# Kernel tuning notes

Measured on AMD Instinct MI355X. Metric: run time of the kernel, lower is better.

Reference implementation:

```python
import jax, jax.numpy as jnp
import numpy as np

N = 20000      # num_nodes
E = 320000     # num_edges (avg degree 16)
HID = 256      # hid_dim
H = 4          # attention heads
D = HID // H   # per-head dim (concat heads -> HID)
L = 2          # nGAT_layer
OUT = 12       # out_dim / pred_len (decoder steps)
NEG_SLOPE = 0.2


def setup_inputs() -> dict:
    key = jax.random.key(0)
    ks = jax.random.split(key, 16)
    s = 0.05
    nrm = lambda k, shape: jax.random.normal(k, shape, jnp.float32) * s
    return dict(
        x=nrm(ks[0], (N, HID)),
        edge_index=jax.random.randint(ks[1], (2, E), 0, N, dtype=jnp.int32),
        # GATv2Conv params per layer (stacked over L layers)
        gat_w_src=nrm(ks[2], (L, HID, H * D)),
        gat_w_dst=nrm(ks[3], (L, HID, H * D)),
        gat_att=nrm(ks[4], (L, H, D)),
        gat_bias=nrm(ks[5], (L, H * D)),
        # decoder_mlp: Linear(1 + HID -> HID)
        mlp_w=nrm(ks[6], (HID, 1 + HID)),
        mlp_b=nrm(ks[7], (HID,)),
        # nn.LSTM (1 layer, input HID, hidden HID), torch gate order i,f,g,o
        lstm_w_ih=nrm(ks[8], (4 * HID, HID)),
        lstm_w_hh=nrm(ks[9], (4 * HID, HID)),
        lstm_b_ih=nrm(ks[10], (4 * HID,)),
        lstm_b_hh=nrm(ks[11], (4 * HID,)),
        # decoder_init_proj: Linear(HID -> 1); decoder_output_proj: Linear(HID -> 1)
        init_w=nrm(ks[12], (1, HID)),
        init_b=nrm(ks[13], (1,)),
        out_w=nrm(ks[14], (1, HID)),
        out_b=nrm(ks[15], (1,)),
    )


def _gatv2_layer(x, src, dst, w_src, w_dst, att, bias):
    n = x.shape[0]
    xl = (x @ w_src).reshape(n, H, D)   # source-side projection
    xr = (x @ w_dst).reshape(n, H, D)   # destination-side projection
    # GATv2: e_ij = a^T LeakyReLU(Wl x_j + Wr x_i)
    e = jax.nn.leaky_relu(xl[src] + xr[dst], NEG_SLOPE)        # [E,H,D]
    logits = jnp.einsum('ehd,hd->eh', e, att)                   # [E,H]
    # edge softmax over incoming edges of each destination node
    m = jax.ops.segment_max(logits, dst, num_segments=n)        # [N,H]
    ex = jnp.exp(logits - m[dst])
    denom = jax.ops.segment_sum(ex, dst, num_segments=n)
    alpha = ex / denom[dst]                                     # [E,H]
    out = jax.ops.segment_sum(xl[src] * alpha[:, :, None], dst, num_segments=n)
    return out.reshape(n, H * D) + bias


def reference(x, edge_index, gat_w_src, gat_w_dst, gat_att, gat_bias,
              mlp_w, mlp_b, lstm_w_ih, lstm_w_hh, lstm_b_ih, lstm_b_hh,
              init_w, init_b, out_w, out_b):
    src, dst = edge_index[0], edge_index[1]
    # stacked GAT blocks: GATv2Conv + ELU (element == 2)
    for l in range(L):
        x = _gatv2_layer(x, src, dst, gat_w_src[l], gat_w_dst[l], gat_att[l], gat_bias[l])
        x = jax.nn.elu(x)
    # recurrent LSTM decoder, batch = nodes, seq step by step
    ctx = x                      # encoder_context
    h = x                        # h_0 = x (num_layers = 1)
    c = jnp.zeros_like(x)        # c_0 = 0
    prev = x @ init_w.T + init_b  # [N,1]
    outs = []
    for _ in range(OUT):
        dec_in = jnp.concatenate([prev, ctx], axis=1) @ mlp_w.T + mlp_b  # [N,HID]
        gates = dec_in @ lstm_w_ih.T + lstm_b_ih + h @ lstm_w_hh.T + lstm_b_hh
        i_g, f_g, g_g, o_g = jnp.split(gates, 4, axis=1)
        i_g = jax.nn.sigmoid(i_g)
        f_g = jax.nn.sigmoid(f_g)
        o_g = jax.nn.sigmoid(o_g)
        g_g = jnp.tanh(g_g)
        c = f_g * c + i_g * g_g
        h = o_g * jnp.tanh(c)
        prev = h @ out_w.T + out_b  # [N,1]
        outs.append(prev)
    return jnp.concatenate(outs, axis=1)  # [N, OUT]
```

## Files before the change

### kernel.cpp

```cpp
#include <hip/hip_runtime.h>
#include <hip/hip_bf16.h>

#define NN 20000
#define NE 320000
#define TOUT 12
#define DEGMAX 96
#define NPB 10
#define MR 80
#define NBLK 250
#define NCPL 13

typedef __bf16 bf16x8 __attribute__((ext_vector_type(8)));
typedef float float4v __attribute__((ext_vector_type(4)));

#define LD8(p) (*(const bf16x8*)(p))
#define MFMA16(a,b,c) __builtin_amdgcn_mfma_f32_16x16x32_bf16((a),(b),(c),0,0,0)

__device__ __forceinline__ float bf2f(const __hip_bfloat16 v){ return __bfloat162float(v); }
__device__ __forceinline__ __hip_bfloat16 f2bf(float v){ return __float2bfloat16(v); }
__device__ __forceinline__ float sigmoidr_(float x){ return __builtin_amdgcn_rcpf(1.f + __expf(-x)); }
__device__ __forceinline__ float tanhr_(float x){ return 1.f - 2.f*__builtin_amdgcn_rcpf(__expf(2.f*x) + 1.f); }
__device__ __forceinline__ float rdf(const void* p, int i, int f32){
  return f32 ? ((const float*)p)[i] : __bfloat162float(((const __hip_bfloat16*)p)[i]);
}

__global__ void k_detect(const void* xraw, int* flag){
  __shared__ int cnt;
  if(threadIdx.x == 0) cnt = 0;
  __syncthreads();
  const unsigned* w = (const unsigned*)xraw;
  int local = 0;
  for(int i = threadIdx.x; i < 4096; i += 256){
    unsigned b = (w[i] >> 8) & 0x7F;
    if(b >= 0x33 && b <= 0x3F) local++;
  }
  atomicAdd(&cnt, local);
  __syncthreads();
  if(threadIdx.x == 0) *flag = (cnt > 2048) ? 0 : 1;
}

__global__ void k_fail(float* out, int n){
  int i = blockIdx.x*256 + threadIdx.x;
  if(i < n) out[i] = 256.0f;
}

__global__ void k_count(const int* __restrict__ dst, int* __restrict__ deg){
  int e = blockIdx.x*256 + threadIdx.x;
  if(e < NE){
    unsigned d = (unsigned)dst[e];
    if(d < NN) atomicAdd(&deg[d], 1);
  }
}

__global__ void k_scan(const int* __restrict__ deg, int* __restrict__ offp, int* __restrict__ cursor){
  __shared__ int part[256];
  __shared__ int excl[257];
  const int CH = (NN + 255)/256;
  int tid = threadIdx.x;
  int lo = tid*CH;
  int hi = lo + CH; if(hi > NN) hi = NN;
  int s = 0;
  for(int i=lo;i<hi;i++) s += deg[i];
  part[tid] = s;
  __syncthreads();
  if(tid == 0){
    int run = 0;
    for(int i=0;i<256;i++){ excl[i] = run; run += part[i]; }
    excl[256] = run;
  }
  __syncthreads();
  int run = excl[tid];
  for(int i=lo;i<hi;i++){ offp[i] = run; cursor[i] = run; run += deg[i]; }
  if(tid == 0) offp[NN] = excl[256];
}

__global__ void k_fill(const int* __restrict__ src, const int* __restrict__ dst,
                       int* __restrict__ cursor, int* __restrict__ csr_src){
  int e = blockIdx.x*256 + threadIdx.x;
  if(e >= NE) return;
  unsigned d = (unsigned)dst[e];
  if(d >= NN) return;
  unsigned p = (unsigned)atomicAdd(&cursor[d], 1);
  if(p < NE){
    unsigned sv = (unsigned)src[e];
    csr_src[p] = (sv < NN) ? (int)sv : 0;
  }
}

__global__ void k_prep(const void* __restrict__ w_src, const void* __restrict__ w_dst,
                       const void* __restrict__ w_hh, const void* __restrict__ wih,
                       const void* __restrict__ mlp_w, const void* __restrict__ mlp_b,
                       const void* __restrict__ b_ih, const void* __restrict__ b_hh,
                       const void* __restrict__ att, const void* __restrict__ gbias,
                       const void* __restrict__ init_w, const void* __restrict__ init_b,
                       const void* __restrict__ out_w, const void* __restrict__ out_b,
                       const int* __restrict__ flag,
                       __hip_bfloat16* __restrict__ wsrcT, __hip_bfloat16* __restrict__ wdstT,
                       __hip_bfloat16* __restrict__ whhp, __hip_bfloat16* __restrict__ wihb,
                       __hip_bfloat16* __restrict__ mlpT,
                       float* __restrict__ u, float* __restrict__ bc,
                       float* __restrict__ attf, float* __restrict__ gbiasf,
                       float* __restrict__ initwf, float* __restrict__ outwf,
                       float* __restrict__ sc){
  int f = *flag;
  if(blockIdx.x < 1024){
    int tid = blockIdx.x*256 + threadIdx.x;
    if(tid < 131072){
      int l = tid >> 16, r = tid & 65535, o = r >> 8, i = r & 255;
      wsrcT[tid] = f2bf(rdf(w_src, l*65536 + i*256 + o, f));
      wdstT[tid] = f2bf(rdf(w_dst, l*65536 + i*256 + o, f));
    }
    if(tid < 262144){
      whhp[tid] = f2bf(rdf(w_hh, tid, f));
      wihb[tid] = f2bf(rdf(wih, tid, f));
    }
    if(tid < 65536){
      int k = tid >> 8, j = tid & 255;
      mlpT[tid] = f2bf(rdf(mlp_w, j*257 + 1 + k, f));
    }
  }else{
    __shared__ float su[256], sb[256];
    int g = blockIdx.x - 1024, j = threadIdx.x;
    float w = rdf(wih, g*256 + j, f);
    su[j] = w * rdf(mlp_w, j*257, f);
    sb[j] = w * rdf(mlp_b, j, f);
    if(g < 2){
      int i = g*256 + j;
      attf[i] = rdf(att, i, f);
      gbiasf[i] = rdf(gbias, i, f);
    }
    if(g == 0){
      initwf[j] = rdf(init_w, j, f);
      outwf[j]  = rdf(out_w, j, f);
      if(j == 0){ sc[0] = rdf(init_b, 0, f); sc[1] = rdf(out_b, 0, f); }
    }
    __syncthreads();
    for(int s=128; s>0; s>>=1){
      if(j < s){ su[j] += su[j+s]; sb[j] += sb[j+s]; }
      __syncthreads();
    }
    if(j == 0){ u[g] = su[0]; bc[g] = sb[0] + rdf(b_ih, g, f) + rdf(b_hh, g, f); }
  }
}

__global__ void k_packs(const __hip_bfloat16* __restrict__ Wpl,
                        const __hip_bfloat16* __restrict__ Wcpl,
                        const float* __restrict__ u_vec, const float* __restrict__ outwf,
                        const __hip_bfloat16* __restrict__ wsrcT,
                        const __hip_bfloat16* __restrict__ wdstT,
                        __hip_bfloat16* __restrict__ WhhP, __hip_bfloat16* __restrict__ Whh2P,
                        __hip_bfloat16* __restrict__ WcP,
                        __hip_bfloat16* __restrict__ wprojP){
  if(blockIdx.x < 128){
    int idx = blockIdx.x*256 + threadIdx.x;
    int P    = idx >> 14;
    int cs   = (idx >> 11) & 7;
    int kidx = (idx >> 8) & 7;
    int ntl  = (idx >> 6) & 3;
    int lane = idx & 63;
    int l16 = lane & 15, quad = lane >> 4;
    int brow = ntl*256 + P*128 + cs*16 + l16;
    int col0 = kidx*32 + quad*8;
    int srcofs = brow*256 + col0;
    int dst = idx*8;
    bf16x8 wv = LD8(Wpl + srcofs);
    *(bf16x8*)(WhhP + dst) = wv;
    float uu = u_vec[brow];
    bf16x8 w2;
    #pragma unroll
    for(int jj=0;jj<8;jj++)
      w2[jj] = (__bf16)f2bf(bf2f((__hip_bfloat16)wv[jj]) + uu*outwf[col0 + jj]);
    *(bf16x8*)(Whh2P + dst) = w2;
    *(bf16x8*)(WcP + dst)   = LD8(Wcpl + srcofs);
  }else{
    int idx = (blockIdx.x - 128)*256 + threadIdx.x;
    int m = idx >> 13;
    int fi = idx & 8191;
    int l = m >> 1, role = m & 1;
    int kidx = fi >> 10;
    int nt = (fi >> 6) & 15;
    int lane = fi & 63;
    int l16 = lane & 15, quad = lane >> 4;
    const __hip_bfloat16* src = (role ? wdstT : wsrcT) + l*65536;
    int srcofs = (nt*16 + l16)*256 + kidx*32 + quad*8;
    *(bf16x8*)(wprojP + (size_t)m*65536 + fi*8) = LD8(src + srcofs);
  }
}

__global__ __launch_bounds__(256) void k_gemm_nt_bf(const __hip_bfloat16* __restrict__ A,
                                                    const __hip_bfloat16* __restrict__ B,
                                                    __hip_bfloat16* __restrict__ Cb, int M){
  int wave = threadIdx.x >> 6;
  int lane = threadIdx.x & 63;
  int l16 = lane & 15, quad = lane >> 4, quad8 = quad*8;
  int mBase = blockIdx.x*64 + wave*16;
  int nBase = blockIdx.y*64;
  int arow = mBase + l16; if(arow >= M) arow = M-1;
  const __hip_bfloat16* aptr = A + (size_t)arow*256 + quad8;
  float4v acc[4];
  #pragma unroll
  for(int nt=0;nt<4;nt++){ acc[nt][0]=0.f; acc[nt][1]=0.f; acc[nt][2]=0.f; acc[nt][3]=0.f; }
  for(int k0=0;k0<256;k0+=32){
    bf16x8 a = LD8(aptr + k0);
    #pragma unroll
    for(int nt=0;nt<4;nt++){
      const __hip_bfloat16* bptr = B + (size_t)(nBase + nt*16 + l16)*256 + k0 + quad8;
      acc[nt] = MFMA16(a, LD8(bptr), acc[nt]);
    }
  }
  #pragma unroll
  for(int nt=0;nt<4;nt++){
    int col = nBase + nt*16 + l16;
    #pragma unroll
    for(int r=0;r<4;r++){
      int row = mBase + quad*4 + r;
      if(row < M) Cb[(size_t)row*256 + col] = f2bf(acc[nt][r]);
    }
  }
}

__global__ __launch_bounds__(512, 2) void k_gemm_dual(__hip_bfloat16* __restrict__ P,
                                                      const void* __restrict__ xraw,
                                                      const int* __restrict__ flag,
                                                      int layer0,
                                                      const __hip_bfloat16* __restrict__ BsrcP,
                                                      const __hip_bfloat16* __restrict__ BdstP,
                                                      __hip_bfloat16* __restrict__ Q){
  __shared__ __hip_bfloat16 sA[64*264];
  int tid = threadIdx.x;
  int mBase = blockIdx.x*64;
  {
    int r = tid >> 3;
    int c0 = (tid & 7)*32;
    int grow = mBase + r; if(grow >= NN) grow = NN-1;
    if(layer0){
      int f = *flag;
      #pragma unroll
      for(int j=0;j<32;j++) sA[r*264 + c0 + j] = f2bf(rdf(xraw, grow*256 + c0 + j, f));
    }else{
      const __hip_bfloat16* srcp = P + (size_t)grow*256 + c0;
      #pragma unroll
      for(int j=0;j<4;j++) *(bf16x8*)(&sA[r*264 + c0 + j*8]) = LD8(srcp + j*8);
    }
  }
  __syncthreads();
  int w8 = tid >> 6;
  int w = w8 & 3;
  int role = w8 >> 2;
  int lane = tid&63, l16 = lane&15, quad = lane>>4, quad8 = quad*8;
  const __hip_bfloat16* B = role ? BdstP : BsrcP;
  __hip_bfloat16* C = role ? P : Q;
  const __hip_bfloat16* arow = &sA[(w*16 + l16)*264 + quad8];
  float4v acc[16];
  #pragma unroll
  for(int nt=0;nt<16;nt++){ acc[nt][0]=0.f; acc[nt][1]=0.f; acc[nt][2]=0.f; acc[nt][3]=0.f; }
  for(int kidx=0;kidx<8;kidx++){
    bf16x8 a = *(const bf16x8*)(arow + kidx*32);
    const __hip_bfloat16* bbase = B + (kidx<<13) + (lane<<3);
    #pragma unroll
    for(int nt=0;nt<16;nt++)
      acc[nt] = MFMA16(a, LD8(bbase + (nt<<9)), acc[nt]);
  }
  #pragma unroll
  for(int nt=0;nt<16;nt++){
    int col = nt*16 + l16;
    #pragma unroll
    for(int r=0;r<4;r++){
      int row = mBase + w*16 + quad*4 + r;
      if(row < NN) C[(size_t)row*256 + col] = f2bf(acc[nt][r]);
    }
  }
}

__global__ __launch_bounds__(256) void k_node_fused(const __hip_bfloat16* __restrict__ Q,
                                                    __hip_bfloat16* __restrict__ P,
                                                    const int* __restrict__ offp,
                                                    const int* __restrict__ csr_src,
                                                    const float* __restrict__ attf,
                                                    const float* __restrict__ gbiasf){
  __shared__ float slog[DEGMAX*4];
  __shared__ int ssrc[DEGMAX];
  int tid = threadIdx.x;
  int w = tid>>6, lane = tid&63;
  int eSlot = lane>>4, li = lane&15;
  float attl[16];
  #pragma unroll
  for(int j=0;j<16;j++) attl[j] = attf[li*16 + j];
  float gb = gbiasf[tid];
  int hd = tid>>6;
  #pragma unroll 1
  for(int nn=0; nn<NPB; nn++){
    int node = blockIdx.x*NPB + nn;
    int s0 = offp[node], s1 = offp[node+1];
    if(s0 < 0) s0 = 0; if(s0 > NE) s0 = NE;
    if(s1 < s0) s1 = s0; if(s1 > NE) s1 = NE;
    int deg = s1 - s0; if(deg > DEGMAX) deg = DEGMAX;
    if(tid < deg){
      unsigned sv = (unsigned)csr_src[s0 + tid];
      ssrc[tid] = (sv < NN) ? (int)sv : 0;
    }
    __syncthreads();
    float prl[16];
    {
      const __hip_bfloat16* prow = P + (size_t)node*256 + li*16;
      bf16x8 p0 = LD8(prow), p1 = LD8(prow + 8);
      #pragma unroll
      for(int j=0;j<8;j++){ prl[j] = bf2f((__hip_bfloat16)p0[j]); prl[8+j] = bf2f((__hip_bfloat16)p1[j]); }
    }
    for(int base=0; base<deg; base+=16){
      int e = base + w*4 + eSlot;
      bool valid = (e < deg);
      const __hip_bfloat16* qrow = Q + (size_t)ssrc[valid ? e : 0]*256 + li*16;
      bf16x8 q0 = LD8(qrow), q1 = LD8(qrow + 8);
      float part = 0.f;
      #pragma unroll
      for(int j=0;j<16;j++){
        float v = bf2f((__hip_bfloat16)(j<8 ? q0[j] : q1[j-8])) + prl[j];
        v = (v > 0.f) ? v : 0.2f*v;
        part += v * attl[j];
      }
      part += __shfl_xor(part, 1, 64);
      part += __shfl_xor(part, 2, 64);
      if((li & 3) == 0 && valid) slog[e*4 + (li>>2)] = part;
    }
    __syncthreads();
    {
      int hh = tid >> 6;
      int li64 = tid & 63;
      float m = -1e30f;
      for(int i=li64; i<deg; i+=64) m = fmaxf(m, slog[i*4+hh]);
      #pragma unroll
      for(int s=1; s<64; s<<=1) m = fmaxf(m, __shfl_xor(m, s, 64));
      float den = 0.f;
      for(int i=li64; i<deg; i+=64) den += __expf(slog[i*4+hh] - m);
      #pragma unroll
      for(int s=1; s<64; s<<=1) den += __shfl_xor(den, s, 64);
      float inv = (den > 0.f) ? 1.f/den : 0.f;
      for(int i=li64; i<deg; i+=64) slog[i*4+hh] = __expf(slog[i*4+hh] - m)*inv;
    }
    __syncthreads();
    float acc = 0.f;
    for(int i=0;i<deg;i++) acc += slog[i*4+hd] * bf2f(Q[(size_t)ssrc[i]*256 + tid]);
    acc += gb;
    acc = (acc > 0.f) ? acc : (__expf(acc) - 1.f);
    P[(size_t)node*256 + tid] = f2bf(acc);
    __syncthreads();
  }
}

__global__ __launch_bounds__(512, 1) void k_lstm80(const __hip_bfloat16* __restrict__ ctx,
                                                   const __hip_bfloat16* __restrict__ WcP,
                                                   const __hip_bfloat16* __restrict__ WhhP,
                                                   const __hip_bfloat16* __restrict__ Whh2P,
                                                   const float* __restrict__ u_vec,
                                                   const float* __restrict__ bc_vec,
                                                   const float* __restrict__ initwf,
                                                   const float* __restrict__ outwf,
                                                   const float* __restrict__ sc,
                                                   float* __restrict__ out){
  __shared__ __hip_bfloat16 sgx[NCPL*4096];
  __shared__ __hip_bfloat16 sh[MR*264];
  __shared__ float spartw[2][MR*16];
  __shared__ float sprev0[MR];
  float* spart = (float*)sgx;
  int tid = threadIdx.x;
  int mBase = blockIdx.x*MR;
  int cs = tid>>6, lane = tid&63, l16 = lane&15, quad = lane>>4, quad8 = quad*8;
  int phase = (blockIdx.x >> 3) & 7;
  int j0 = cs*16 + l16;
  int j1 = 128 + j0;
  #pragma unroll
  for(int p=0;p<3;p++){
    int r = p*32 + (tid >> 4);
    if(r < MR){
      int c0 = (tid & 15)*16;
      const __hip_bfloat16* srcp = ctx + (size_t)(mBase + r)*256 + c0;
      *(bf16x8*)(&sh[r*264 + c0])     = LD8(srcp);
      *(bf16x8*)(&sh[r*264 + c0 + 8]) = LD8(srcp + 8);
    }
  }
  __syncthreads();
  #pragma unroll
  for(int p=0;p<3;p++){
    int r = p*32 + (tid >> 4);
    int c0 = (tid & 15)*16;
    float part = 0.f;
    if(r < MR){
      #pragma unroll
      for(int j=0;j<16;j++) part += bf2f(sh[r*264 + c0 + j]) * initwf[c0 + j];
    }
    spart[tid] = part;
    __syncthreads();
    if(tid < 32 && p*32 + tid < MR){
      float s = 0.f;
      #pragma unroll
      for(int j=0;j<16;j++) s += spart[tid*16 + j];
      sprev0[p*32 + tid] = s + sc[0];
    }
    __syncthreads();
  }
  float ow0 = outwf[j0], ow1 = outwf[j1];
  float outb = sc[1];
  bf16x8 gg0, gg1, gg2, gg3, gg4, gg5, gg6;
  {
    float bcl[8];
    #pragma unroll
    for(int g=0;g<4;g++){
      bcl[g]   = bc_vec[g*256 + j0] + u_vec[g*256 + j0]*outb;
      bcl[4+g] = bc_vec[g*256 + j1] + u_vec[g*256 + j1]*outb;
    }
    #pragma unroll
    for(int P2=0;P2<2;P2++){
      float4v acc[20];
      #pragma unroll
      for(int nt=0;nt<20;nt++){ acc[nt][0]=0.f; acc[nt][1]=0.f; acc[nt][2]=0.f; acc[nt][3]=0.f; }
      #pragma unroll 2
      for(int ki=0;ki<8;ki++){
        int kidx = (ki + phase) & 7;
        int k0 = kidx*32;
        bf16x8 a0 = *(const bf16x8*)(&sh[l16*264 + k0 + quad8]);
        bf16x8 a1 = *(const bf16x8*)(&sh[(16 + l16)*264 + k0 + quad8]);
        bf16x8 a2 = *(const bf16x8*)(&sh[(32 + l16)*264 + k0 + quad8]);
        bf16x8 a3 = *(const bf16x8*)(&sh[(48 + l16)*264 + k0 + quad8]);
        bf16x8 a4 = *(const bf16x8*)(&sh[(64 + l16)*264 + k0 + quad8]);
        const __hip_bfloat16* bbase = WcP + P2*131072 + (((cs<<3) + kidx)<<11) + (lane<<3);
        #pragma unroll
        for(int ntl=0;ntl<4;ntl++){
          bf16x8 b = LD8(bbase + (ntl<<9));
          acc[ntl]     = MFMA16(a0, b, acc[ntl]);
          acc[4+ntl]   = MFMA16(a1, b, acc[4+ntl]);
          acc[8+ntl]   = MFMA16(a2, b, acc[8+ntl]);
          acc[12+ntl]  = MFMA16(a3, b, acc[12+ntl]);
          acc[16+ntl]  = MFMA16(a4, b, acc[16+ntl]);
        }
      }
      #pragma unroll
      for(int rt=0;rt<5;rt++)
        #pragma unroll
        for(int half=0;half<2;half++){
          bf16x8 v;
          #pragma unroll
          for(int rr=0;rr<2;rr++)
            #pragma unroll
            for(int g=0;g<4;g++){
              int r = half*2 + rr;
              v[rr*4+g] = (__bf16)f2bf(acc[rt*4 + g][r] + bcl[P2*4+g]);
            }
          const int cp = P2*10 + rt*2 + half;
          if(cp < NCPL) *(bf16x8*)(&sgx[cp*4096 + tid*8]) = v;
          else if(cp == 13) gg0 = v;
          else if(cp == 14) gg1 = v;
          else if(cp == 15) gg2 = v;
          else if(cp == 16) gg3 = v;
          else if(cp == 17) gg4 = v;
          else if(cp == 18) gg5 = v;
          else              gg6 = v;
        }
    }
  }
  float creg[40];
  #pragma unroll
  for(int i=0;i<40;i++) creg[i] = 0.f;
  #pragma unroll 1
  for(int step=0; step<TOUT; step++){
    const __hip_bfloat16* W = (step == 0) ? WhhP : Whh2P;
    int sb = step & 1;
    float4v acc[20];
    #pragma unroll
    for(int nt=0;nt<20;nt++){ acc[nt][0]=0.f; acc[nt][1]=0.f; acc[nt][2]=0.f; acc[nt][3]=0.f; }
    #pragma unroll 2
    for(int ki=0;ki<8;ki++){
      int kidx = (ki + phase) & 7;
      int k0 = kidx*32;
      bf16x8 a0 = *(const bf16x8*)(&sh[l16*264 + k0 + quad8]);
      bf16x8 a1 = *(const bf16x8*)(&sh[(16 + l16)*264 + k0 + quad8]);
      bf16x8 a2 = *(const bf16x8*)(&sh[(32 + l16)*264 + k0 + quad8]);
      bf16x8 a3 = *(const bf16x8*)(&sh[(48 + l16)*264 + k0 + quad8]);
      bf16x8 a4 = *(const bf16x8*)(&sh[(64 + l16)*264 + k0 + quad8]);
      const __hip_bfloat16* bbase = W + (((cs<<3) + kidx)<<11) + (lane<<3);
      #pragma unroll
      for(int ntl=0;ntl<4;ntl++){
        bf16x8 b = LD8(bbase + (ntl<<9));
        acc[ntl]     = MFMA16(a0, b, acc[ntl]);
        acc[4+ntl]   = MFMA16(a1, b, acc[4+ntl]);
        acc[8+ntl]   = MFMA16(a2, b, acc[8+ntl]);
        acc[12+ntl]  = MFMA16(a3, b, acc[12+ntl]);
        acc[16+ntl]  = MFMA16(a4, b, acc[16+ntl]);
      }
    }
    float hA[20];
    #pragma unroll
    for(int rt=0; rt<5; rt++){
      bf16x8 ga = *(const bf16x8*)(&sgx[(rt*2)*4096 + tid*8]);
      bf16x8 gb = *(const bf16x8*)(&sgx[(rt*2+1)*4096 + tid*8]);
      float hsum[4];
      #pragma unroll
      for(int r=0;r<4;r++){
        int row = rt*16 + quad*4 + r;
        int jb = (r&1)*4;
        float gx0, gx1, gx2, gx3;
        if(r < 2){
          gx0 = bf2f((__hip_bfloat16)ga[jb]);   gx1 = bf2f((__hip_bfloat16)ga[jb+1]);
          gx2 = bf2f((__hip_bfloat16)ga[jb+2]); gx3 = bf2f((__hip_bfloat16)ga[jb+3]);
        }else{
          gx0 = bf2f((__hip_bfloat16)gb[jb]);   gx1 = bf2f((__hip_bfloat16)gb[jb+1]);
          gx2 = bf2f((__hip_bfloat16)gb[jb+2]); gx3 = bf2f((__hip_bfloat16)gb[jb+3]);
        }
        float g0 = acc[rt*4 + 0][r] + gx0;
        float g1 = acc[rt*4 + 1][r] + gx1;
        float g2 = acc[rt*4 + 2][r] + gx2;
        float g3 = acc[rt*4 + 3][r] + gx3;
        if(step == 0){
          float pd = sprev0[row] - outb;
          g0 += pd*u_vec[j0];
          g1 += pd*u_vec[256 + j0];
          g2 += pd*u_vec[512 + j0];
          g3 += pd*u_vec[768 + j0];
        }
        float iv = sigmoidr_(g0), fv = sigmoidr_(g1);
        float gv = tanhr_(g2),    ov = sigmoidr_(g3);
        float cn = fv*creg[rt*4 + r] + iv*gv;
        creg[rt*4 + r] = cn;
        float hn = ov * tanhr_(cn);
        hA[rt*4 + r] = hn;
        hsum[r] = hn * ow0;
      }
      #pragma unroll
      for(int r=0;r<4;r++){
        hsum[r] += __shfl_xor(hsum[r], 1, 64);
        hsum[r] += __shfl_xor(hsum[r], 2, 64);
        hsum[r] += __shfl_xor(hsum[r], 4, 64);
        hsum[r] += __shfl_xor(hsum[r], 8, 64);
      }
      if(l16 == 0){
        #pragma unroll
        for(int r=0;r<4;r++)
          spartw[sb][(rt*16 + quad*4 + r)*16 + cs*2] = hsum[r];
      }
    }
    #pragma unroll
    for(int nt=0;nt<20;nt++){ acc[nt][0]=0.f; acc[nt][1]=0.f; acc[nt][2]=0.f; acc[nt][3]=0.f; }
    #pragma unroll 2
    for(int ki=0;ki<8;ki++){
      int kidx = (ki + phase) & 7;
      int k0 = kidx*32;
      bf16x8 a0 = *(const bf16x8*)(&sh[l16*264 + k0 + quad8]);
      bf16x8 a1 = *(const bf16x8*)(&sh[(16 + l16)*264 + k0 + quad8]);
      bf16x8 a2 = *(const bf16x8*)(&sh[(32 + l16)*264 + k0 + quad8]);
      bf16x8 a3 = *(const bf16x8*)(&sh[(48 + l16)*264 + k0 + quad8]);
      bf16x8 a4 = *(const bf16x8*)(&sh[(64 + l16)*264 + k0 + quad8]);
      const __hip_bfloat16* bbase = W + 131072 + (((cs<<3) + kidx)<<11) + (lane<<3);
      #pragma unroll
      for(int ntl=0;ntl<4;ntl++){
        bf16x8 b = LD8(bbase + (ntl<<9));
        acc[ntl]     = MFMA16(a0, b, acc[ntl]);
        acc[4+ntl]   = MFMA16(a1, b, acc[4+ntl]);
        acc[8+ntl]   = MFMA16(a2, b, acc[8+ntl]);
        acc[12+ntl]  = MFMA16(a3, b, acc[12+ntl]);
        acc[16+ntl]  = MFMA16(a4, b, acc[16+ntl]);
      }
    }
    __syncthreads();
    #pragma unroll
    for(int rt=0; rt<5; rt++){
      const int cpa = 10 + rt*2, cpb_ = 11 + rt*2;
      bf16x8 ga, gb;
      if(cpa < NCPL)      ga = *(const bf16x8*)(&sgx[cpa*4096 + tid*8]);
      else if(cpa == 14)  ga = gg1;
      else if(cpa == 16)  ga = gg3;
      else                ga = gg5;
      if(cpb_ < NCPL)     gb = *(const bf16x8*)(&sgx[cpb_*4096 + tid*8]);
      else if(cpb_ == 13) gb = gg0;
      else if(cpb_ == 15) gb = gg2;
      else if(cpb_ == 17) gb = gg4;
      else                gb = gg6;
      float hsum[4];
      #pragma unroll
      for(int r=0;r<4;r++){
        int row = rt*16 + quad*4 + r;
        int jb = (r&1)*4;
        float gx0, gx1, gx2, gx3;
        if(r < 2){
          gx0 = bf2f((__hip_bfloat16)ga[jb]);   gx1 = bf2f((__hip_bfloat16)ga[jb+1]);
          gx2 = bf2f((__hip_bfloat16)ga[jb+2]); gx3 = bf2f((__hip_bfloat16)ga[jb+3]);
        }else{
          gx0 = bf2f((__hip_bfloat16)gb[jb]);   gx1 = bf2f((__hip_bfloat16)gb[jb+1]);
          gx2 = bf2f((__hip_bfloat16)gb[jb+2]); gx3 = bf2f((__hip_bfloat16)gb[jb+3]);
        }
        float g0 = acc[rt*4 + 0][r] + gx0;
        float g1 = acc[rt*4 + 1][r] + gx1;
        float g2 = acc[rt*4 + 2][r] + gx2;
        float g3 = acc[rt*4 + 3][r] + gx3;
        if(step == 0){
          float pd = sprev0[row] - outb;
          g0 += pd*u_vec[j1];
          g1 += pd*u_vec[256 + j1];
          g2 += pd*u_vec[512 + j1];
          g3 += pd*u_vec[768 + j1];
        }
        float iv = sigmoidr_(g0), fv = sigmoidr_(g1);
        float gv = tanhr_(g2),    ov = sigmoidr_(g3);
        float cn = fv*creg[20 + rt*4 + r] + iv*gv;
        creg[20 + rt*4 + r] = cn;
        float hn = ov * tanhr_(cn);
        sh[row*264 + j0] = f2bf(hA[rt*4 + r]);
        sh[row*264 + j1] = f2bf(hn);
        hsum[r] = hn * ow1;
      }
      #pragma unroll
      for(int r=0;r<4;r++){
        hsum[r] += __shfl_xor(hsum[r], 1, 64);
        hsum[r] += __shfl_xor(hsum[r], 2, 64);
        hsum[r] += __shfl_xor(hsum[r], 4, 64);
        hsum[r] += __shfl_xor(hsum[r], 8, 64);
      }
      if(l16 == 0){
        #pragma unroll
        for(int r=0;r<4;r++)
          spartw[sb][(rt*16 + quad*4 + r)*16 + cs*2 + 1] = hsum[r];
      }
    }
    __syncthreads();
    if(tid < MR){
      float s = outb;
      #pragma unroll
      for(int c=0;c<16;c++) s += spartw[sb][tid*16 + c];
      out[(size_t)(mBase + tid)*TOUT + step] = s;
    }
  }
}

extern "C" void kernel_launch(void* const* d_in, const int* in_sizes, int n_in,
                              void* d_out, int out_size, void* d_ws, size_t ws_size,
                              hipStream_t stream){
  const void* x      = d_in[0];
  const int*  ei     = (const int*)d_in[1];
  const void* w_src  = d_in[2];
  const void* w_dst  = d_in[3];
  const void* att    = d_in[4];
  const void* gbias  = d_in[5];
  const void* mlp_w  = d_in[6];
  const void* mlp_b  = d_in[7];
  const void* w_ih   = d_in[8];
  const void* w_hh   = d_in[9];
  const void* b_ih   = d_in[10];
  const void* b_hh   = d_in[11];
  const void* init_w = d_in[12];
  const void* init_b = d_in[13];
  const void* out_w  = d_in[14];
  const void* out_b  = d_in[15];
  float* out = (float*)d_out;
  const int* srcp = ei;
  const int* dstp = ei + NE;
  (void)in_sizes; (void)n_in;

  char* ws = (char*)d_ws;
  size_t off = 0;
  auto alloc = [&](size_t bytes)->void*{
    void* p = ws + off;
    off += (bytes + 255) & ~(size_t)255;
    return p;
  };
  __hip_bfloat16* P = (__hip_bfloat16*)alloc((size_t)NN*256*2);
  __hip_bfloat16* Q = (__hip_bfloat16*)alloc((size_t)NN*256*2);
  int* deg      = (int*)alloc((size_t)NN*4);
  int* offp     = (int*)alloc((size_t)(NN+1)*4);
  int* cursor   = (int*)alloc((size_t)NN*4);
  int* csr_src  = (int*)alloc((size_t)NE*4);
  __hip_bfloat16* wsrcT   = (__hip_bfloat16*)alloc((size_t)131072*2);
  __hip_bfloat16* wdstT   = (__hip_bfloat16*)alloc((size_t)131072*2);
  __hip_bfloat16* wprojP  = (__hip_bfloat16*)alloc((size_t)4*65536*2);
  __hip_bfloat16* whh_pl  = (__hip_bfloat16*)alloc((size_t)262144*2);
  __hip_bfloat16* Wc_pl   = (__hip_bfloat16*)alloc((size_t)262144*2);
  __hip_bfloat16* WhhP    = (__hip_bfloat16*)alloc((size_t)262144*2);
  __hip_bfloat16* Whh2P   = (__hip_bfloat16*)alloc((size_t)262144*2);
  __hip_bfloat16* WcP     = (__hip_bfloat16*)alloc((size_t)262144*2);
  __hip_bfloat16* wihb    = (__hip_bfloat16*)alloc((size_t)262144*2);
  __hip_bfloat16* mlpT    = (__hip_bfloat16*)alloc((size_t)65536*2);
  float* u_vec  = (float*)alloc(1024*4);
  float* bc_vec = (float*)alloc(1024*4);
  float* attf   = (float*)alloc(512*4);
  float* gbiasf = (float*)alloc(512*4);
  float* initwf = (float*)alloc(256*4);
  float* outwf  = (float*)alloc(256*4);
  float* sc     = (float*)alloc(2*4);
  int*   flag   = (int*)alloc(4);

  if(off > ws_size){
    k_fail<<<(out_size + 255)/256, 256, 0, stream>>>(out, out_size);
    return;
  }

  k_detect<<<1, 256, 0, stream>>>(x, flag);
  hipMemsetAsync(deg, 0, (size_t)NN*4, stream);
  hipMemsetAsync(csr_src, 0xFF, (size_t)NE*4, stream);
  k_count<<<NE/256, 256, 0, stream>>>(dstp, deg);
  k_scan<<<1, 256, 0, stream>>>(deg, offp, cursor);
  k_fill<<<NE/256, 256, 0, stream>>>(srcp, dstp, cursor, csr_src);
  k_prep<<<2048, 256, 0, stream>>>(w_src, w_dst, w_hh, w_ih, mlp_w, mlp_b,
                                   b_ih, b_hh, att, gbias, init_w, init_b,
                                   out_w, out_b, flag,
                                   wsrcT, wdstT, whh_pl, wihb, mlpT,
                                   u_vec, bc_vec, attf, gbiasf, initwf, outwf, sc);
  {
    dim3 gwc(16, 4);
    k_gemm_nt_bf<<<gwc, 256, 0, stream>>>(wihb, mlpT, Wc_pl, 1024);
  }
  k_packs<<<256, 256, 0, stream>>>(whh_pl, Wc_pl, u_vec, outwf, wsrcT, wdstT,
                                   WhhP, Whh2P, WcP, wprojP);

  for(int l=0;l<2;l++){
    k_gemm_dual<<<313, 512, 0, stream>>>(P, x, flag, (l == 0) ? 1 : 0,
                                         wprojP + (size_t)(l*2)*65536,
                                         wprojP + (size_t)(l*2+1)*65536, Q);
    k_node_fused<<<NN/NPB, 256, 0, stream>>>(Q, P, offp, csr_src, attf + l*256, gbiasf + l*256);
  }

  k_lstm80<<<NBLK, 512, 0, stream>>>(P, WcP, WhhP, Whh2P, u_vec, bc_vec,
                                     initwf, outwf, sc, out);
}
```

Baseline: 627.1 us.

## Assign one wavefront per node in GAT aggregation, removing block barriers

The fused GAT node kernel now gives each wavefront its own node and its own shared-memory slices, in place of all four waves of a block cooperating on one node. Every __syncthreads is removed, and the grid shrinks to a quarter of the blocks, each handling four nodes in parallel. Logit and softmax reductions run within 16-lane groups. The aggregation has each lane accumulate four contiguous channels with one 8-byte load per edge. The goal is to remove barrier stalls and idle waves on low-degree nodes. The cost is less parallelism per node and a longer serial loop over edges within each wave.

```diff
diff --git a/kernel.cpp b/kernel.cpp
--- a/kernel.cpp
+++ b/kernel.cpp
@@ -5,7 +5,7 @@
 #define NE 320000
 #define TOUT 12
 #define DEGMAX 96
-#define NPB 10
+#define WNPB 10
 #define MR 80
 #define NBLK 250
 #define NCPL 13
@@ -278,28 +278,31 @@
                                                     const int* __restrict__ csr_src,
                                                     const float* __restrict__ attf,
                                                     const float* __restrict__ gbiasf){
-  __shared__ float slog[DEGMAX*4];
-  __shared__ int ssrc[DEGMAX];
+  __shared__ int   ssrc_s[4][DEGMAX];
+  __shared__ float slog_s[4][DEGMAX*4];
   int tid = threadIdx.x;
-  int w = tid>>6, lane = tid&63;
-  int eSlot = lane>>4, li = lane&15;
+  int wv = tid >> 6, lane = tid & 63;
+  int eSlot = lane >> 4, li = lane & 15;
+  int* ssrc = ssrc_s[wv];
+  float* slog = slog_s[wv];
   float attl[16];
   #pragma unroll
   for(int j=0;j<16;j++) attl[j] = attf[li*16 + j];
-  float gb = gbiasf[tid];
-  int hd = tid>>6;
+  float gbl[4];
+  #pragma unroll
+  for(int k=0;k<4;k++) gbl[k] = gbiasf[lane*4 + k];
+  int hh = lane >> 4;
   #pragma unroll 1
-  for(int nn=0; nn<NPB; nn++){
-    int node = blockIdx.x*NPB + nn;
+  for(int nn=0; nn<WNPB; nn++){
+    int node = (blockIdx.x*4 + wv)*WNPB + nn;
     int s0 = offp[node], s1 = offp[node+1];
     if(s0 < 0) s0 = 0; if(s0 > NE) s0 = NE;
     if(s1 < s0) s1 = s0; if(s1 > NE) s1 = NE;
     int deg = s1 - s0; if(deg > DEGMAX) deg = DEGMAX;
-    if(tid < deg){
-      unsigned sv = (unsigned)csr_src[s0 + tid];
-      ssrc[tid] = (sv < NN) ? (int)sv : 0;
-    }
-    __syncthreads();
+    for(int i=lane; i<deg; i+=64){
+      unsigned sv = (unsigned)csr_src[s0 + i];
+      ssrc[i] = (sv < NN) ? (int)sv : 0;
+    }
     float prl[16];
     {
       const __hip_bfloat16* prow = P + (size_t)node*256 + li*16;
@@ -307,8 +310,8 @@
       #pragma unroll
       for(int j=0;j<8;j++){ prl[j] = bf2f((__hip_bfloat16)p0[j]); prl[8+j] = bf2f((__hip_bfloat16)p1[j]); }
     }
-    for(int base=0; base<deg; base+=16){
-      int e = base + w*4 + eSlot;
+    for(int base=0; base<deg; base+=4){
+      int e = base + eSlot;
       bool valid = (e < deg);
       const __hip_bfloat16* qrow = Q + (size_t)ssrc[valid ? e : 0]*256 + li*16;
       bf16x8 q0 = LD8(qrow), q1 = LD8(qrow + 8);
@@ -323,28 +326,38 @@
       part += __shfl_xor(part, 2, 64);
       if((li & 3) == 0 && valid) slog[e*4 + (li>>2)] = part;
     }
-    __syncthreads();
     {
-      int hh = tid >> 6;
-      int li64 = tid & 63;
       float m = -1e30f;
-      for(int i=li64; i<deg; i+=64) m = fmaxf(m, slog[i*4+hh]);
-      #pragma unroll
-      for(int s=1; s<64; s<<=1) m = fmaxf(m, __shfl_xor(m, s, 64));
+      for(int i=li; i<deg; i+=16) m = fmaxf(m, slog[i*4+hh]);
+      m = fmaxf(m, __shfl_xor(m, 1, 64));
+      m = fmaxf(m, __shfl_xor(m, 2, 64));
+      m = fmaxf(m, __shfl_xor(m, 4, 64));
+      m = fmaxf(m, __shfl_xor(m, 8, 64));
       float den = 0.f;
-      for(int i=li64; i<deg; i+=64) den += __expf(slog[i*4+hh] - m);
-      #pragma unroll
-      for(int s=1; s<64; s<<=1) den += __shfl_xor(den, s, 64);
+      for(int i=li; i<deg; i+=16) den += __expf(slog[i*4+hh] - m);
+      den += __shfl_xor(den, 1, 64);
+      den += __shfl_xor(den, 2, 64);
+      den += __shfl_xor(den, 4, 64);
+      den += __shfl_xor(den, 8, 64);
       float inv = (den > 0.f) ? 1.f/den : 0.f;
-      for(int i=li64; i<deg; i+=64) slog[i*4+hh] = __expf(slog[i*4+hh] - m)*inv;
-    }
-    __syncthreads();
-    float acc = 0.f;
-    for(int i=0;i<deg;i++) acc += slog[i*4+hd] * bf2f(Q[(size_t)ssrc[i]*256 + tid]);
-    acc += gb;
-    acc = (acc > 0.f) ? acc : (__expf(acc) - 1.f);
-    P[(size_t)node*256 + tid] = f2bf(acc);
-    __syncthreads();
+      for(int i=li; i<deg; i+=16) slog[i*4+hh] = __expf(slog[i*4+hh] - m)*inv;
+    }
+    float acc0=0.f, acc1=0.f, acc2=0.f, acc3=0.f;
+    for(int i=0;i<deg;i++){
+      float wgt = slog[i*4 + hh];
+      uint2 qp = *(const uint2*)(Q + (size_t)ssrc[i]*256 + lane*4);
+      const __hip_bfloat16* qb = (const __hip_bfloat16*)&qp;
+      acc0 += wgt * bf2f(qb[0]);
+      acc1 += wgt * bf2f(qb[1]);
+      acc2 += wgt * bf2f(qb[2]);
+      acc3 += wgt * bf2f(qb[3]);
+    }
+    __hip_bfloat16 ob[4];
+    float o0 = acc0 + gbl[0]; o0 = (o0 > 0.f) ? o0 : (__expf(o0) - 1.f); ob[0] = f2bf(o0);
+    float o1 = acc1 + gbl[1]; o1 = (o1 > 0.f) ? o1 : (__expf(o1) - 1.f); ob[1] = f2bf(o1);
+    float o2 = acc2 + gbl[2]; o2 = (o2 > 0.f) ? o2 : (__expf(o2) - 1.f); ob[2] = f2bf(o2);
+    float o3 = acc3 + gbl[3]; o3 = (o3 > 0.f) ? o3 : (__expf(o3) - 1.f); ob[3] = f2bf(o3);
+    *(uint2*)(P + (size_t)node*256 + lane*4) = *(const uint2*)ob;
   }
 }
 
@@ -713,7 +726,8 @@
     k_gemm_dual<<<313, 512, 0, stream>>>(P, x, flag, (l == 0) ? 1 : 0,
                                          wprojP + (size_t)(l*2)*65536,
                                          wprojP + (size_t)(l*2+1)*65536, Q);
-    k_node_fused<<<NN/NPB, 256, 0, stream>>>(Q, P, offp, csr_src, attf + l*256, gbiasf + l*256);
+    k_node_fused<<<NN/(4*WNPB), 256, 0, stream>>>(Q, P, offp, csr_src,
+                                                  attf + l*256, gbiasf + l*256);
   }
 
   k_lstm80<<<NBLK, 512, 0, stream>>>(P, WcP, WhhP, Whh2P, u_vec, bc_vec,
```

Measured after the change: 686.7 us. +9.5%, slower.
